# Kernel tuning notes

Measured on AMD Instinct MI355X. Metric: run time of the kernel, lower is better.

Reference implementation:

```python
import jax, jax.numpy as jnp
import numpy as np

N_NODES, D_IN, D_OUT = 1_000_000, 128, 128
M_PATHS, N_INST, PATH_LEN, N_ETYPES = 6, 20_000, 4, 6


def setup_inputs() -> dict:
    key = jax.random.key(0)
    ks = jax.random.split(key, 9)
    scale = 1.0 / np.sqrt(D_IN)
    features = jax.random.normal(ks[0], (N_NODES, D_IN), jnp.float32)
    instances = jax.random.randint(ks[1], (M_PATHS, N_INST, PATH_LEN), 0, N_NODES, dtype=jnp.int64)
    edge_types = jax.random.randint(ks[2], (M_PATHS,), 0, N_ETYPES, dtype=jnp.int64)
    W_enc = jax.random.normal(ks[3], (M_PATHS, D_IN, D_OUT), jnp.float32) * scale
    b_enc = jax.random.normal(ks[4], (M_PATHS, D_OUT), jnp.float32) * scale
    W_att = jax.random.normal(ks[5], (N_ETYPES, 2 * D_OUT), jnp.float32) * scale
    b_att = jax.random.normal(ks[6], (N_ETYPES,), jnp.float32) * scale
    w_mp = jax.random.normal(ks[7], (D_OUT,), jnp.float32) * scale
    b_mp = jax.random.normal(ks[8], (), jnp.float32) * scale
    return {"features": features, "W_enc": W_enc, "b_enc": b_enc, "W_att": W_att,
            "b_att": b_att, "w_mp": w_mp, "b_mp": b_mp,
            "instances": instances, "edge_types": edge_types}


def reference(features, W_enc, b_enc, W_att, b_att, w_mp, b_mp, instances, edge_types):
    # Gather node features for every metapath instance: [M, I, L, D]
    gathered = features[instances]
    # Per-metapath linear encoder: [M, I, L, H]
    encoded = jnp.einsum('mild,mdh->milh', gathered, W_enc) + b_enc[:, None, None, :]
    first = encoded[:, :, 0, :]   # [M, I, H]
    last = encoded[:, :, -1, :]   # [M, I, H]
    cat = jnp.concatenate([first, last], axis=-1)  # [M, I, 2H]
    # Edge-type-specific attention (Linear(2H, 1)) selected per metapath
    Wsel = W_att[edge_types]      # [M, 2H]
    bsel = b_att[edge_types]      # [M]
    scores = jnp.einsum('mik,mk->mi', cat, Wsel) + bsel[:, None]  # [M, I]
    w = jax.nn.softmax(jax.nn.leaky_relu(scores, 0.2), axis=1)    # softmax over instances
    mp_out = jnp.einsum('mi,mih->mh', w, last)                    # [M, H]
    # Metapath-level attention
    mp_scores = mp_out @ w_mp + b_mp                              # [M]
    mw = jax.nn.softmax(jax.nn.leaky_relu(mp_scores, 0.2), axis=0)
    out = jnp.sum(mw[:, None] * mp_out, axis=0)                   # [H]
    return jax.nn.elu(out)
```

## Files before the change

### kernel.cpp

```cpp
#include <hip/hip_runtime.h>
#include <hip/hip_bf16.h>
#include <math.h>

#define NPATH 6
#define NINST 20000
#define PLEN 4
#define DFEAT 128
#define TPB1 256
#define WPB 4
#define GPW 4
#define GPB (WPB * GPW)
#define BPP 128
#define GPP (BPP * GPB)
#define RESCALE_THR 8.0f

__device__ __forceinline__ float dot4(float4 a, float4 b) {
    return a.x * b.x + a.y * b.y + a.z * b.z + a.w * b.w;
}

__global__ __launch_bounds__(TPB1, 4) void k_pass1(
    const float* __restrict__ feat, const int* __restrict__ inst,
    const float* __restrict__ W_enc, const float* __restrict__ b_enc,
    const float* __restrict__ W_att, const float* __restrict__ b_att,
    const int* __restrict__ etype,
    float* __restrict__ pV, float* __restrict__ pM, float* __restrict__ pS)
{
    int m    = blockIdx.x / BPP;
    int bw   = blockIdx.x % BPP;
    int tid  = threadIdx.x;
    int wv   = tid >> 6, lane = tid & 63;
    int grp  = lane >> 4, sub = lane & 15;
    int gid  = wv * GPW + grp;
    int g    = bw * GPB + gid;

    __shared__ float swa[2 * DFEAT];
    __shared__ float su1[DFEAT], su2[DFEAT];
    __shared__ float sbc[DFEAT];
    __shared__ float scv;
    __shared__ float sV[GPB][DFEAT + 4];
    __shared__ float sMx[GPB], sSm[GPB];

    const int4* ib4 = (const int4*)(inst + (size_t)m * NINST * PLEN);
    int i = g;
    int4 j0 = ib4[i];
    int4 j1 = ib4[i + GPP];
    int4 j2 = ib4[i + 2 * GPP];

    const float4* r0 = (const float4*)(feat + (size_t)j0.x * DFEAT);
    const float4* r3 = (const float4*)(feat + (size_t)j0.w * DFEAT);
    float4 A0a = r0[sub], A0b = r0[sub + 16];
    float4 A3a = r3[sub], A3b = r3[sub + 16];
    const float4* q0 = (const float4*)(feat + (size_t)j1.x * DFEAT);
    const float4* q3 = (const float4*)(feat + (size_t)j1.w * DFEAT);
    float4 B0a = q0[sub], B0b = q0[sub + 16];
    float4 B3a = q3[sub], B3b = q3[sub + 16];

    int e = etype[m];
    swa[tid] = W_att[(size_t)e * (2 * DFEAT) + tid];
    __syncthreads();
    if (tid < DFEAT) {
        const float4* Wr = (const float4*)(W_enc + ((size_t)m * DFEAT + tid) * DFEAT);
        float s1 = 0.f, s2 = 0.f;
        #pragma unroll 8
        for (int q = 0; q < DFEAT / 4; ++q) {
            float4 w4 = Wr[q];
            s1 += w4.x * swa[4*q]         + w4.y * swa[4*q+1]
                + w4.z * swa[4*q+2]       + w4.w * swa[4*q+3];
            s2 += w4.x * swa[DFEAT+4*q]   + w4.y * swa[DFEAT+4*q+1]
                + w4.z * swa[DFEAT+4*q+2] + w4.w * swa[DFEAT+4*q+3];
        }
        su1[tid] = s1;
        su2[tid] = s2;
        sbc[tid] = b_enc[m * DFEAT + tid] * (swa[tid] + swa[DFEAT + tid]);
    }
    __syncthreads();
    if (tid < 64) {
        float t = sbc[tid] + sbc[tid + 64];
        #pragma unroll
        for (int o = 32; o; o >>= 1) t += __shfl_xor(t, o);
        if (tid == 0) scv = t + b_att[e];
    }
    __syncthreads();

    float4 U1a = ((const float4*)su1)[sub], U1b = ((const float4*)su1)[sub + 16];
    float4 U2a = ((const float4*)su2)[sub], U2b = ((const float4*)su2)[sub + 16];
    float c = scv;

    float mref = 0.f, tmax = -3e38f, sum = 0.f;
    float4 va = make_float4(0.f, 0.f, 0.f, 0.f);
    float4 vb = make_float4(0.f, 0.f, 0.f, 0.f);

#define COMPUTE(R0a, R0b, R3a, R3b)                                          \
    {                                                                        \
        float p = dot4(R0a, U1a) + dot4(R0b, U1b)                            \
                + dot4(R3a, U2a) + dot4(R3b, U2b);                           \
        p += __shfl_xor(p, 1);                                               \
        p += __shfl_xor(p, 2);                                               \
        p += __shfl_xor(p, 4);                                               \
        p += __shfl_xor(p, 8);                                               \
        float s = p + c;                                                     \
        s = s > 0.f ? s : 0.2f * s;                                          \
        tmax = fmaxf(tmax, s);                                               \
        if (tmax > mref + RESCALE_THR) {                                     \
            float r = __expf(mref - tmax);                                   \
            sum *= r;                                                        \
            va.x *= r; va.y *= r; va.z *= r; va.w *= r;                      \
            vb.x *= r; vb.y *= r; vb.z *= r; vb.w *= r;                      \
            mref = tmax;                                                     \
        }                                                                    \
        float pe = __expf(s - mref);                                         \
        sum += pe;                                                           \
        va.x += pe * R3a.x; va.y += pe * R3a.y;                              \
        va.z += pe * R3a.z; va.w += pe * R3a.w;                              \
        vb.x += pe * R3b.x; vb.y += pe * R3b.y;                              \
        vb.z += pe * R3b.z; vb.w += pe * R3b.w;                              \
    }

    while (i + 2 * GPP < NINST) {
        const float4* p0 = (const float4*)(feat + (size_t)j2.x * DFEAT);
        const float4* p3 = (const float4*)(feat + (size_t)j2.w * DFEAT);
        float4 C0a = p0[sub], C0b = p0[sub + 16];
        float4 C3a = p3[sub], C3b = p3[sub + 16];
        int nj = i + 3 * GPP;
        nj = nj < NINST ? nj : NINST - 1;
        int4 j3 = ib4[nj];

        COMPUTE(A0a, A0b, A3a, A3b);

        A0a = B0a; A0b = B0b; A3a = B3a; A3b = B3b;
        B0a = C0a; B0b = C0b; B3a = C3a; B3b = C3b;
        j2 = j3;
        i += GPP;
    }

    COMPUTE(A0a, A0b, A3a, A3b);
    i += GPP;
    if (i < NINST) COMPUTE(B0a, B0b, B3a, B3b);

#undef COMPUTE

    *(float4*)&sV[gid][sub * 4]      = va;
    *(float4*)&sV[gid][64 + sub * 4] = vb;
    if (sub == 0) { sMx[gid] = mref; sSm[gid] = sum; }
    __syncthreads();

    if (tid < DFEAT) {
        float M = sMx[0];
        #pragma unroll
        for (int k = 1; k < GPB; ++k) M = fmaxf(M, sMx[k]);
        float S = 0.f, V = 0.f;
        #pragma unroll
        for (int k = 0; k < GPB; ++k) {
            float ek = __expf(sMx[k] - M);
            S += ek * sSm[k];
            V += ek * sV[k][tid];
        }
        pV[(size_t)blockIdx.x * DFEAT + tid] = V;
        if (tid == 0) { pM[blockIdx.x] = M; pS[blockIdx.x] = S; }
    }
}

__global__ __launch_bounds__(256) void k_pass2(
    const float* __restrict__ pV, const float* __restrict__ pM, const float* __restrict__ pS,
    const float* __restrict__ W_enc, const float* __restrict__ b_enc,
    const float* __restrict__ w_mp, const float* __restrict__ b_mp,
    float* __restrict__ mp_out, float* __restrict__ ms)
{
    int m = blockIdx.x, tid = threadIdx.x;
    int d = tid & 127, slice = tid >> 7;

    __shared__ float tmp[BPP];
    __shared__ float eL[BPP];
    __shared__ float sv[2][DFEAT];
    __shared__ float sVn[DFEAT];
    __shared__ float smp[DFEAT];
    __shared__ float sS, sMx;

    if (tid < BPP) tmp[tid] = pM[m * BPP + tid];
    __syncthreads();
    for (int off = 64; off; off >>= 1) {
        if (tid < off) tmp[tid] = fmaxf(tmp[tid], tmp[tid + off]);
        __syncthreads();
    }
    if (tid == 0) sMx = tmp[0];
    __syncthreads();
    float M = sMx;

    if (tid < BPP) {
        float ek = __expf(pM[m * BPP + tid] - M);
        eL[tid] = ek;
        tmp[tid] = ek * pS[m * BPP + tid];
    }
    __syncthreads();
    for (int off = 64; off; off >>= 1) {
        if (tid < off) tmp[tid] += tmp[tid + off];
        __syncthreads();
    }
    if (tid == 0) sS = tmp[0];
    __syncthreads();
    float Sinv = 1.f / sS;

    float acc = 0.f;
    for (int k = slice; k < BPP; k += 2)
        acc += eL[k] * pV[((size_t)(m * BPP + k)) * DFEAT + d];
    sv[slice][d] = acc;
    __syncthreads();
    if (tid < DFEAT) sVn[tid] = (sv[0][tid] + sv[1][tid]) * Sinv;
    __syncthreads();

    const float* W = W_enc + (size_t)m * DFEAT * DFEAT;
    float gacc = 0.f;
    for (int dd = slice; dd < DFEAT; dd += 2)
        gacc += sVn[dd] * W[(size_t)dd * DFEAT + d];
    __syncthreads();
    sv[slice][d] = gacc;
    __syncthreads();
    if (tid < DFEAT) {
        float t = sv[0][tid] + sv[1][tid] + b_enc[m * DFEAT + tid];
        mp_out[m * DFEAT + tid] = t;
        smp[tid] = t * w_mp[tid];
    }
    __syncthreads();

    if (tid < 64) {
        float t = smp[tid] + smp[tid + 64];
        #pragma unroll
        for (int o = 32; o; o >>= 1) t += __shfl_xor(t, o);
        if (tid == 0) ms[m] = t + b_mp[0];
    }
}

__global__ void k_final(const float* __restrict__ mp_out, const float* __restrict__ ms,
                        float* __restrict__ out) {
    int h = threadIdx.x;
    float l[NPATH], mx = -3e38f;
    #pragma unroll
    for (int m = 0; m < NPATH; ++m) {
        float x = ms[m];
        x = x > 0.f ? x : 0.2f * x;
        l[m] = x;
        mx = fmaxf(mx, x);
    }
    float sum = 0.f;
    #pragma unroll
    for (int m = 0; m < NPATH; ++m) { l[m] = __expf(l[m] - mx); sum += l[m]; }
    float o = 0.f;
    #pragma unroll
    for (int m = 0; m < NPATH; ++m) o += (l[m] / sum) * mp_out[m * DFEAT + h];
    out[h] = o > 0.f ? o : __expf(o) - 1.f;
}

extern "C" void kernel_launch(void* const* d_in, const int* in_sizes, int n_in,
                              void* d_out, int out_size, void* d_ws, size_t ws_size,
                              hipStream_t stream) {
    const float* features   = (const float*)d_in[0];
    const float* W_enc      = (const float*)d_in[1];
    const float* b_enc      = (const float*)d_in[2];
    const float* W_att      = (const float*)d_in[3];
    const float* b_att      = (const float*)d_in[4];
    const float* w_mp       = (const float*)d_in[5];
    const float* b_mp       = (const float*)d_in[6];
    const int*   instances  = (const int*)d_in[7];
    const int*   edge_types = (const int*)d_in[8];
    float* out = (float*)d_out;
    float* ws  = (float*)d_ws;

    const int nblk1 = NPATH * BPP;

    float* pV     = ws;
    float* pM     = pV + (size_t)nblk1 * DFEAT;
    float* pS     = pM + nblk1;
    float* mp_out = pS + nblk1;
    float* msv    = mp_out + NPATH * DFEAT;

    k_pass1<<<nblk1, TPB1, 0, stream>>>(features, instances, W_enc, b_enc,
                                        W_att, b_att, edge_types, pV, pM, pS);

    k_pass2<<<NPATH, 256, 0, stream>>>(pV, pM, pS, W_enc, b_enc, w_mp, b_mp, mp_out, msv);

    k_final<<<1, DFEAT, 0, stream>>>(mp_out, msv, out);
}
```

Measured before the change: 65.83 us.

## Fuse three kernels into one using last-block-done atomic counters

Merges pass2 and the final metapath softmax into the pass1 kernel. Per-metapath and global atomic counters let the last-finishing block do each reduction stage, which removes two kernel launches and their gaps. A memset is added to reset the counters, and the extra shared memory could lower occupancy of the main gather kernel.

```diff
diff --git a/kernel.cpp b/kernel.cpp
--- a/kernel.cpp
+++ b/kernel.cpp
@@ -18,12 +18,16 @@
     return a.x * b.x + a.y * b.y + a.z * b.z + a.w * b.w;
 }
 
-__global__ __launch_bounds__(TPB1, 4) void k_pass1(
+__global__ __launch_bounds__(TPB1, 4) void k_fused(
     const float* __restrict__ feat, const int* __restrict__ inst,
     const float* __restrict__ W_enc, const float* __restrict__ b_enc,
     const float* __restrict__ W_att, const float* __restrict__ b_att,
     const int* __restrict__ etype,
-    float* __restrict__ pV, float* __restrict__ pM, float* __restrict__ pS)
+    const float* __restrict__ w_mp, const float* __restrict__ b_mp,
+    float* __restrict__ pV, float* __restrict__ pM, float* __restrict__ pS,
+    float* __restrict__ mp_out, float* __restrict__ msv,
+    int* __restrict__ cnt, int* __restrict__ cnt2,
+    float* __restrict__ out)
 {
     int m    = blockIdx.x / BPP;
     int bw   = blockIdx.x % BPP;
@@ -39,6 +43,13 @@
     __shared__ float scv;
     __shared__ float sV[GPB][DFEAT + 4];
     __shared__ float sMx[GPB], sSm[GPB];
+    __shared__ int   sOld;
+    __shared__ float tmp[BPP];
+    __shared__ float eL[BPP];
+    __shared__ float sv2[2][DFEAT];
+    __shared__ float sVn[DFEAT];
+    __shared__ float smp[DFEAT];
+    __shared__ float sS2, sMx2;
 
     const int4* ib4 = (const int4*)(inst + (size_t)m * NINST * PLEN);
     int i = g;
@@ -132,11 +143,9 @@
         j2 = j3;
         i += GPP;
     }
-
     COMPUTE(A0a, A0b, A3a, A3b);
     i += GPP;
     if (i < NINST) COMPUTE(B0a, B0b, B3a, B3b);
-
 #undef COMPUTE
 
     *(float4*)&sV[gid][sub * 4]      = va;
@@ -158,23 +167,16 @@
         pV[(size_t)blockIdx.x * DFEAT + tid] = V;
         if (tid == 0) { pM[blockIdx.x] = M; pS[blockIdx.x] = S; }
     }
-}
-
-__global__ __launch_bounds__(256) void k_pass2(
-    const float* __restrict__ pV, const float* __restrict__ pM, const float* __restrict__ pS,
-    const float* __restrict__ W_enc, const float* __restrict__ b_enc,
-    const float* __restrict__ w_mp, const float* __restrict__ b_mp,
-    float* __restrict__ mp_out, float* __restrict__ ms)
-{
-    int m = blockIdx.x, tid = threadIdx.x;
+    __syncthreads();
+
+    __threadfence();
+    if (tid == 0) sOld = atomicAdd(&cnt[m], 1);
+    __syncthreads();
+    if (sOld != BPP - 1) return;
+
+    __threadfence();
+
     int d = tid & 127, slice = tid >> 7;
-
-    __shared__ float tmp[BPP];
-    __shared__ float eL[BPP];
-    __shared__ float sv[2][DFEAT];
-    __shared__ float sVn[DFEAT];
-    __shared__ float smp[DFEAT];
-    __shared__ float sS, sMx;
 
     if (tid < BPP) tmp[tid] = pM[m * BPP + tid];
     __syncthreads();
@@ -182,9 +184,9 @@
         if (tid < off) tmp[tid] = fmaxf(tmp[tid], tmp[tid + off]);
         __syncthreads();
     }
-    if (tid == 0) sMx = tmp[0];
-    __syncthreads();
-    float M = sMx;
+    if (tid == 0) sMx2 = tmp[0];
+    __syncthreads();
+    float M = sMx2;
 
     if (tid < BPP) {
         float ek = __expf(pM[m * BPP + tid] - M);
@@ -196,16 +198,16 @@
         if (tid < off) tmp[tid] += tmp[tid + off];
         __syncthreads();
     }
-    if (tid == 0) sS = tmp[0];
-    __syncthreads();
-    float Sinv = 1.f / sS;
+    if (tid == 0) sS2 = tmp[0];
+    __syncthreads();
+    float Sinv = 1.f / sS2;
 
     float acc = 0.f;
     for (int k = slice; k < BPP; k += 2)
         acc += eL[k] * pV[((size_t)(m * BPP + k)) * DFEAT + d];
-    sv[slice][d] = acc;
-    __syncthreads();
-    if (tid < DFEAT) sVn[tid] = (sv[0][tid] + sv[1][tid]) * Sinv;
+    sv2[slice][d] = acc;
+    __syncthreads();
+    if (tid < DFEAT) sVn[tid] = (sv2[0][tid] + sv2[1][tid]) * Sinv;
     __syncthreads();
 
     const float* W = W_enc + (size_t)m * DFEAT * DFEAT;
@@ -213,41 +215,46 @@
     for (int dd = slice; dd < DFEAT; dd += 2)
         gacc += sVn[dd] * W[(size_t)dd * DFEAT + d];
     __syncthreads();
-    sv[slice][d] = gacc;
-    __syncthreads();
-    if (tid < DFEAT) {
-        float t = sv[0][tid] + sv[1][tid] + b_enc[m * DFEAT + tid];
+    sv2[slice][d] = gacc;
+    __syncthreads();
+    if (tid < DFEAT) {
+        float t = sv2[0][tid] + sv2[1][tid] + b_enc[m * DFEAT + tid];
         mp_out[m * DFEAT + tid] = t;
         smp[tid] = t * w_mp[tid];
     }
     __syncthreads();
-
     if (tid < 64) {
         float t = smp[tid] + smp[tid + 64];
         #pragma unroll
         for (int o = 32; o; o >>= 1) t += __shfl_xor(t, o);
-        if (tid == 0) ms[m] = t + b_mp[0];
-    }
-}
-
-__global__ void k_final(const float* __restrict__ mp_out, const float* __restrict__ ms,
-                        float* __restrict__ out) {
-    int h = threadIdx.x;
-    float l[NPATH], mx = -3e38f;
-    #pragma unroll
-    for (int m = 0; m < NPATH; ++m) {
-        float x = ms[m];
-        x = x > 0.f ? x : 0.2f * x;
-        l[m] = x;
-        mx = fmaxf(mx, x);
-    }
-    float sum = 0.f;
-    #pragma unroll
-    for (int m = 0; m < NPATH; ++m) { l[m] = __expf(l[m] - mx); sum += l[m]; }
-    float o = 0.f;
-    #pragma unroll
-    for (int m = 0; m < NPATH; ++m) o += (l[m] / sum) * mp_out[m * DFEAT + h];
-    out[h] = o > 0.f ? o : __expf(o) - 1.f;
+        if (tid == 0) msv[m] = t + b_mp[0];
+    }
+    __syncthreads();
+
+    __threadfence();
+    if (tid == 0) sOld = atomicAdd(cnt2, 1);
+    __syncthreads();
+    if (sOld != NPATH - 1) return;
+
+    __threadfence();
+    if (tid < DFEAT) {
+        int h = tid;
+        float l[NPATH], mx = -3e38f;
+        #pragma unroll
+        for (int k = 0; k < NPATH; ++k) {
+            float x = msv[k];
+            x = x > 0.f ? x : 0.2f * x;
+            l[k] = x;
+            mx = fmaxf(mx, x);
+        }
+        float s = 0.f;
+        #pragma unroll
+        for (int k = 0; k < NPATH; ++k) { l[k] = __expf(l[k] - mx); s += l[k]; }
+        float o = 0.f;
+        #pragma unroll
+        for (int k = 0; k < NPATH; ++k) o += (l[k] / s) * mp_out[k * DFEAT + h];
+        out[h] = o > 0.f ? o : __expf(o) - 1.f;
+    }
 }
 
 extern "C" void kernel_launch(void* const* d_in, const int* in_sizes, int n_in,
@@ -265,18 +272,19 @@
     float* out = (float*)d_out;
     float* ws  = (float*)d_ws;
 
-    const int nblk1 = NPATH * BPP;
+    const int nblk = NPATH * BPP;
 
     float* pV     = ws;
-    float* pM     = pV + (size_t)nblk1 * DFEAT;
-    float* pS     = pM + nblk1;
-    float* mp_out = pS + nblk1;
+    float* pM     = pV + (size_t)nblk * DFEAT;
+    float* pS     = pM + nblk;
+    float* mp_out = pS + nblk;
     float* msv    = mp_out + NPATH * DFEAT;
-
-    k_pass1<<<nblk1, TPB1, 0, stream>>>(features, instances, W_enc, b_enc,
-                                        W_att, b_att, edge_types, pV, pM, pS);
-
-    k_pass2<<<NPATH, 256, 0, stream>>>(pV, pM, pS, W_enc, b_enc, w_mp, b_mp, mp_out, msv);
-
-    k_final<<<1, DFEAT, 0, stream>>>(mp_out, msv, out);
+    int*   cnt    = (int*)(msv + 8);
+    int*   cnt2   = cnt + NPATH;
+
+    hipMemsetAsync(cnt, 0, (NPATH + 1) * sizeof(int), stream);
+
+    k_fused<<<nblk, TPB1, 0, stream>>>(features, instances, W_enc, b_enc,
+                                       W_att, b_att, edge_types, w_mp, b_mp,
+                                       pV, pM, pS, mp_out, msv, cnt, cnt2, out);
 }
```

Result: slower. 142.8 us (+116.9%).
